# Kernel tuning notes

Hardware: AMD Instinct MI355X
Metric: run time of the kernel (lower is better)

## Reference

```python
import jax, jax.numpy as jnp
import numpy as np

H = 32  # hidden size
I = 6   # input size


def setup_inputs() -> dict:
    key = jax.random.key(0)
    ks = jax.random.split(key, 10)
    B, T = 8192, 256
    s_i = 1.0 / np.sqrt(H)  # PyTorch LSTM/Linear init scale (uniform), use normal*scale
    return {
        "x": jax.random.normal(ks[0], (B, T, I), dtype=jnp.float32),
        "W_ih": jax.random.normal(ks[1], (4 * H, I), dtype=jnp.float32) * s_i,
        "W_hh": jax.random.normal(ks[2], (4 * H, H), dtype=jnp.float32) * s_i,
        "b_ih": jax.random.normal(ks[3], (4 * H,), dtype=jnp.float32) * s_i,
        "b_hh": jax.random.normal(ks[4], (4 * H,), dtype=jnp.float32) * s_i,
        "W1": jax.random.normal(ks[5], (64, H), dtype=jnp.float32) * s_i,
        "b1": jax.random.normal(ks[6], (64,), dtype=jnp.float32) * s_i,
        "W2": jax.random.normal(ks[7], (1, 64), dtype=jnp.float32) * (1.0 / np.sqrt(64)),
        "b2": jax.random.normal(ks[8], (1,), dtype=jnp.float32) * (1.0 / np.sqrt(64)),
    }


def _lstm_last_h(x, W_ih, W_hh, b_ih, b_hh):
    # x: [B, T, I]. PyTorch gate order: i, f, g, o.
    B = x.shape[0]
    # Precompute input projections for all timesteps: [T, B, 4H]
    xg = jnp.einsum('bti,gi->tbg', x, W_ih) + (b_ih + b_hh)

    def step(carry, xg_t):
        h, c = carry
        gates = xg_t + h @ W_hh.T  # [B, 4H]
        i, f, g, o = jnp.split(gates, 4, axis=-1)
        i = jax.nn.sigmoid(i)
        f = jax.nn.sigmoid(f)
        g = jnp.tanh(g)
        o = jax.nn.sigmoid(o)
        c = f * c + i * g
        h = o * jnp.tanh(c)
        return (h, c), None

    h0 = jnp.zeros((B, H), dtype=x.dtype)
    c0 = jnp.zeros((B, H), dtype=x.dtype)
    (h_last, _), _ = jax.lax.scan(step, (h0, c0), xg)
    return h_last  # == lstm_out[:, -1, :]


def reference(x, W_ih, W_hh, b_ih, b_hh, W1, b1, W2, b2):
    h = _lstm_last_h(x, W_ih, W_hh, b_ih, b_hh)          # [B, 32]
    h = jax.nn.relu(h @ W1.T + b1)                        # [B, 64]
    return h @ W2.T + b2                                  # [B, 1]
```

## Files before the change

### kernel.cpp

```cpp
#include <hip/hip_runtime.h>
#include <cstdint>

#define HSZ 32
#define TSTEPS 256
#define ISZ 6
#define NB 16

typedef _Float16 h8_t __attribute__((ext_vector_type(8)));
typedef float f4_t __attribute__((ext_vector_type(4)));

#if __has_builtin(__builtin_amdgcn_exp2f)
__device__ __forceinline__ float exp2_raw(float x) { return __builtin_amdgcn_exp2f(x); }
#else
__device__ __forceinline__ float exp2_raw(float x) { return __expf(0.69314718056f * x); }
#endif

__global__ __launch_bounds__(64, 2) void lstm_wave(
    const float* __restrict__ x,
    const float* __restrict__ W_ih,
    const float* __restrict__ W_hh,
    const float* __restrict__ b_ih,
    const float* __restrict__ b_hh,
    const float* __restrict__ W1,
    const float* __restrict__ b1,
    const float* __restrict__ W2,
    const float* __restrict__ b2,
    float* __restrict__ out)
{
    __shared__ __align__(16) _Float16 hlds[NB][40];
    __shared__ float w1s[64 * 34];
    __shared__ float b1s[64];
    __shared__ float w2s[64];

    const int lane = threadIdx.x;
    const int n16  = lane & 15;
    const int khi  = lane >> 4;

    for (int i = lane; i < 64 * HSZ; i += 64) w1s[(i >> 5) * 34 + (i & 31)] = W1[i];
    b1s[lane] = b1[lane];
    w2s[lane] = W2[lane];
    #pragma unroll
    for (int i = 0; i < 5; ++i) ((unsigned int*)hlds)[lane + i * 64] = 0u;

    const float LOG2E = 1.44269504f;
    h8_t bhh[8], bih[8];
    f4_t bias4[8];
    #pragma unroll
    for (int q = 0; q < 8; ++q) {
        const int grow = q * 16 + n16;
        const float s = (q == 4 || q == 5) ? (-2.0f * LOG2E) : (-LOG2E);
        const float4* p = (const float4*)(W_hh + grow * HSZ + khi * 8);
        const float4 a = p[0], b = p[1];
        bhh[q][0] = (_Float16)(s * a.x); bhh[q][1] = (_Float16)(s * a.y);
        bhh[q][2] = (_Float16)(s * a.z); bhh[q][3] = (_Float16)(s * a.w);
        bhh[q][4] = (_Float16)(s * b.x); bhh[q][5] = (_Float16)(s * b.y);
        bhh[q][6] = (_Float16)(s * b.z); bhh[q][7] = (_Float16)(s * b.w);
        const float bb = s * (b_ih[grow] + b_hh[grow]);
        bias4[q][0] = bb; bias4[q][1] = bb; bias4[q][2] = bb; bias4[q][3] = bb;
        bih[q][0] = (_Float16)0; bih[q][1] = (_Float16)0;
        bih[q][2] = (_Float16)0; bih[q][3] = (_Float16)0;
        bih[q][4] = (_Float16)0; bih[q][5] = (_Float16)0;
        bih[q][6] = (_Float16)0; bih[q][7] = (_Float16)0;
        if (khi == 0) {
            const float2* pi = (const float2*)(W_ih + grow * ISZ);
            const float2 i0 = pi[0], i1 = pi[1], i2 = pi[2];
            bih[q][0] = (_Float16)(s * i0.x); bih[q][1] = (_Float16)(s * i0.y);
            bih[q][2] = (_Float16)(s * i1.x); bih[q][3] = (_Float16)(s * i1.y);
            bih[q][4] = (_Float16)(s * i2.x); bih[q][5] = (_Float16)(s * i2.y);
        }
    }

    const float* xb = x + (size_t)(blockIdx.x * NB + n16) * (TSTEPS * ISZ);
    float2 xa0 = ((const float2*)xb)[0], xa1 = ((const float2*)xb)[1], xa2 = ((const float2*)xb)[2];
    const float2* pn1 = (const float2*)(xb + ISZ);
    float2 xn0 = pn1[0], xn1 = pn1[1], xn2 = pn1[2];

    float c[2][4] = {{0.f, 0.f, 0.f, 0.f}, {0.f, 0.f, 0.f, 0.f}};

    __builtin_amdgcn_wave_barrier();

    for (int t = 0; t < TSTEPS; ++t) {
        const h8_t ah = *(const h8_t*)&hlds[n16][khi * 8];
        h8_t ax;
        ax[0] = (_Float16)xa0.x; ax[1] = (_Float16)xa0.y;
        ax[2] = (_Float16)xa1.x; ax[3] = (_Float16)xa1.y;
        ax[4] = (_Float16)xa2.x; ax[5] = (_Float16)xa2.y;
        ax[6] = (_Float16)0;     ax[7] = (_Float16)0;
        xa0 = xn0; xa1 = xn1; xa2 = xn2;
        const int tn = (t + 2 < TSTEPS) ? (t + 2) : (TSTEPS - 1);
        const float2* pn = (const float2*)(xb + tn * ISZ);
        xn0 = pn[0]; xn1 = pn[1]; xn2 = pn[2];

        f4_t d[8];
        #pragma unroll
        for (int q = 0; q < 8; ++q)
            d[q] = __builtin_amdgcn_mfma_f32_16x16x32_f16(ax, bih[q], bias4[q], 0, 0, 0);
        #pragma unroll
        for (int q = 0; q < 8; ++q)
            d[q] = __builtin_amdgcn_mfma_f32_16x16x32_f16(ah, bhh[q], d[q], 0, 0, 0);

        #pragma unroll
        for (int hh = 0; hh < 2; ++hh) {
            #pragma unroll
            for (int r = 0; r < 4; ++r) {
                const float iv = __builtin_amdgcn_rcpf(1.0f + exp2_raw(d[0 + hh][r]));
                const float fv = __builtin_amdgcn_rcpf(1.0f + exp2_raw(d[2 + hh][r]));
                const float gv = fmaf(2.0f, __builtin_amdgcn_rcpf(1.0f + exp2_raw(d[4 + hh][r])), -1.0f);
                const float ov = __builtin_amdgcn_rcpf(1.0f + exp2_raw(d[6 + hh][r]));
                c[hh][r] = fmaf(fv, c[hh][r], iv * gv);
                const float th = fmaf(2.0f, __builtin_amdgcn_rcpf(1.0f + exp2_raw(-2.88539008f * c[hh][r])), -1.0f);
                hlds[khi * 4 + r][hh * 16 + n16] = (_Float16)(ov * th);
            }
        }
        __builtin_amdgcn_wave_barrier();
    }

    __builtin_amdgcn_wave_barrier();
    float hr[32];
    #pragma unroll
    for (int q8 = 0; q8 < 4; ++q8) {
        const h8_t hv = *(const h8_t*)&hlds[n16][q8 * 8];
        #pragma unroll
        for (int e = 0; e < 8; ++e) hr[q8 * 8 + e] = (float)hv[e];
    }
    float rsum = 0.0f;
    #pragma unroll
    for (int u = 0; u < 16; ++u) {
        const int row = khi * 16 + u;
        float a = b1s[row];
        #pragma unroll
        for (int k = 0; k < 32; k += 2) {
            const float2 w = *(const float2*)&w1s[row * 34 + k];
            a = fmaf(w.x, hr[k], a);
            a = fmaf(w.y, hr[k + 1], a);
        }
        rsum = fmaf(fmaxf(a, 0.0f), w2s[row], rsum);
    }
    rsum += __shfl_xor(rsum, 16, 64);
    rsum += __shfl_xor(rsum, 32, 64);
    if (khi == 0) out[blockIdx.x * NB + n16] = rsum + b2[0];
}

extern "C" void kernel_launch(void* const* d_in, const int* in_sizes, int n_in,
                              void* d_out, int out_size, void* d_ws, size_t ws_size,
                              hipStream_t stream) {
    const float* x    = (const float*)d_in[0];
    const float* W_ih = (const float*)d_in[1];
    const float* W_hh = (const float*)d_in[2];
    const float* b_ih = (const float*)d_in[3];
    const float* b_hh = (const float*)d_in[4];
    const float* W1   = (const float*)d_in[5];
    const float* b1   = (const float*)d_in[6];
    const float* W2   = (const float*)d_in[7];
    const float* b2   = (const float*)d_in[8];
    float* out = (float*)d_out;

    const int B = in_sizes[0] / (TSTEPS * ISZ);
    const int grid = B / NB;

    lstm_wave<<<grid, 64, 0, stream>>>(x, W_ih, W_hh, b_ih, b_hh,
                                       W1, b1, W2, b2, out);
}
```

Measured before the change: 160.7 us.

## Fold bias into input MFMA, pipeline x-projection, merge sigmoid reciprocals

The combined bias is folded into the input-projection weights through a constant-one column in the x operand, which drops the per-gate bias accumulator registers. The x-projection MFMAs for the next timestep are issued after the gate math of the current one, so they sit off the h-dependent critical path. Sigmoid and tanh products are rewritten to share one reciprocal per pair, with exponents clamped to avoid overflow. This cuts transcendental count per step but adds fp16 rounding of the bias and extra clamp instructions.

```diff
diff --git a/kernel.cpp b/kernel.cpp
--- a/kernel.cpp
+++ b/kernel.cpp
@@ -14,6 +14,7 @@
 #else
 __device__ __forceinline__ float exp2_raw(float x) { return __expf(0.69314718056f * x); }
 #endif
+__device__ __forceinline__ float exp2c(float x) { return exp2_raw(fminf(x, 60.0f)); }
 
 __global__ __launch_bounds__(64, 2) void lstm_wave(
     const float* __restrict__ x,
@@ -44,7 +45,6 @@
 
     const float LOG2E = 1.44269504f;
     h8_t bhh[8], bih[8];
-    f4_t bias4[8];
     #pragma unroll
     for (int q = 0; q < 8; ++q) {
         const int grow = q * 16 + n16;
@@ -55,8 +55,6 @@
         bhh[q][2] = (_Float16)(s * a.z); bhh[q][3] = (_Float16)(s * a.w);
         bhh[q][4] = (_Float16)(s * b.x); bhh[q][5] = (_Float16)(s * b.y);
         bhh[q][6] = (_Float16)(s * b.z); bhh[q][7] = (_Float16)(s * b.w);
-        const float bb = s * (b_ih[grow] + b_hh[grow]);
-        bias4[q][0] = bb; bias4[q][1] = bb; bias4[q][2] = bb; bias4[q][3] = bb;
         bih[q][0] = (_Float16)0; bih[q][1] = (_Float16)0;
         bih[q][2] = (_Float16)0; bih[q][3] = (_Float16)0;
         bih[q][4] = (_Float16)0; bih[q][5] = (_Float16)0;
@@ -67,13 +65,29 @@
             bih[q][0] = (_Float16)(s * i0.x); bih[q][1] = (_Float16)(s * i0.y);
             bih[q][2] = (_Float16)(s * i1.x); bih[q][3] = (_Float16)(s * i1.y);
             bih[q][4] = (_Float16)(s * i2.x); bih[q][5] = (_Float16)(s * i2.y);
+            bih[q][6] = (_Float16)(s * (b_ih[grow] + b_hh[grow]));
         }
     }
 
     const float* xb = x + (size_t)(blockIdx.x * NB + n16) * (TSTEPS * ISZ);
-    float2 xa0 = ((const float2*)xb)[0], xa1 = ((const float2*)xb)[1], xa2 = ((const float2*)xb)[2];
-    const float2* pn1 = (const float2*)(xb + ISZ);
-    float2 xn0 = pn1[0], xn1 = pn1[1], xn2 = pn1[2];
+    float2 xn0 = ((const float2*)xb)[0], xn1 = ((const float2*)xb)[1], xn2 = ((const float2*)xb)[2];
+
+    const f4_t zf = {0.f, 0.f, 0.f, 0.f};
+    h8_t ax;
+    ax[0] = (_Float16)xn0.x; ax[1] = (_Float16)xn0.y;
+    ax[2] = (_Float16)xn1.x; ax[3] = (_Float16)xn1.y;
+    ax[4] = (_Float16)xn2.x; ax[5] = (_Float16)xn2.y;
+    ax[6] = (_Float16)1;     ax[7] = (_Float16)0;
+
+    f4_t dx[8];
+    #pragma unroll
+    for (int q = 0; q < 8; ++q)
+        dx[q] = __builtin_amdgcn_mfma_f32_16x16x32_f16(ax, bih[q], zf, 0, 0, 0);
+
+    {
+        const float2* pn = (const float2*)(xb + ISZ);
+        xn0 = pn[0]; xn1 = pn[1]; xn2 = pn[2];
+    }
 
     float c[2][4] = {{0.f, 0.f, 0.f, 0.f}, {0.f, 0.f, 0.f, 0.f}};
 
@@ -81,37 +95,39 @@
 
     for (int t = 0; t < TSTEPS; ++t) {
         const h8_t ah = *(const h8_t*)&hlds[n16][khi * 8];
-        h8_t ax;
-        ax[0] = (_Float16)xa0.x; ax[1] = (_Float16)xa0.y;
-        ax[2] = (_Float16)xa1.x; ax[3] = (_Float16)xa1.y;
-        ax[4] = (_Float16)xa2.x; ax[5] = (_Float16)xa2.y;
-        ax[6] = (_Float16)0;     ax[7] = (_Float16)0;
-        xa0 = xn0; xa1 = xn1; xa2 = xn2;
-        const int tn = (t + 2 < TSTEPS) ? (t + 2) : (TSTEPS - 1);
-        const float2* pn = (const float2*)(xb + tn * ISZ);
-        xn0 = pn[0]; xn1 = pn[1]; xn2 = pn[2];
-
         f4_t d[8];
         #pragma unroll
         for (int q = 0; q < 8; ++q)
-            d[q] = __builtin_amdgcn_mfma_f32_16x16x32_f16(ax, bih[q], bias4[q], 0, 0, 0);
-        #pragma unroll
-        for (int q = 0; q < 8; ++q)
-            d[q] = __builtin_amdgcn_mfma_f32_16x16x32_f16(ah, bhh[q], d[q], 0, 0, 0);
+            d[q] = __builtin_amdgcn_mfma_f32_16x16x32_f16(ah, bhh[q], dx[q], 0, 0, 0);
 
         #pragma unroll
         for (int hh = 0; hh < 2; ++hh) {
             #pragma unroll
             for (int r = 0; r < 4; ++r) {
-                const float iv = __builtin_amdgcn_rcpf(1.0f + exp2_raw(d[0 + hh][r]));
-                const float fv = __builtin_amdgcn_rcpf(1.0f + exp2_raw(d[2 + hh][r]));
-                const float gv = fmaf(2.0f, __builtin_amdgcn_rcpf(1.0f + exp2_raw(d[4 + hh][r])), -1.0f);
-                const float ov = __builtin_amdgcn_rcpf(1.0f + exp2_raw(d[6 + hh][r]));
-                c[hh][r] = fmaf(fv, c[hh][r], iv * gv);
-                const float th = fmaf(2.0f, __builtin_amdgcn_rcpf(1.0f + exp2_raw(-2.88539008f * c[hh][r])), -1.0f);
-                hlds[khi * 4 + r][hh * 16 + n16] = (_Float16)(ov * th);
+                const float ei = exp2c(d[0 + hh][r]);
+                const float ef = exp2c(d[2 + hh][r]);
+                const float eg = exp2c(d[4 + hh][r]);
+                const float eo = exp2c(d[6 + hh][r]);
+                const float fv = __builtin_amdgcn_rcpf(1.0f + ef);
+                const float ig = (1.0f - eg) * __builtin_amdgcn_rcpf((1.0f + ei) * (1.0f + eg));
+                c[hh][r] = fmaf(fv, c[hh][r], ig);
+                const float ec = exp2c(-2.88539008f * c[hh][r]);
+                const float hv = (1.0f - ec) * __builtin_amdgcn_rcpf((1.0f + eo) * (1.0f + ec));
+                hlds[khi * 4 + r][hh * 16 + n16] = (_Float16)hv;
             }
         }
+
+        ax[0] = (_Float16)xn0.x; ax[1] = (_Float16)xn0.y;
+        ax[2] = (_Float16)xn1.x; ax[3] = (_Float16)xn1.y;
+        ax[4] = (_Float16)xn2.x; ax[5] = (_Float16)xn2.y;
+        #pragma unroll
+        for (int q = 0; q < 8; ++q)
+            dx[q] = __builtin_amdgcn_mfma_f32_16x16x32_f16(ax, bih[q], zf, 0, 0, 0);
+
+        const int tn = (t + 2 < TSTEPS) ? (t + 2) : (TSTEPS - 1);
+        const float2* pn = (const float2*)(xb + tn * ISZ);
+        xn0 = pn[0]; xn1 = pn[1]; xn2 = pn[2];
+
         __builtin_amdgcn_wave_barrier();
     }
 
```

Result: slower. 186.7 us (+16.2%).

## Split LSTM hidden units across two waves with double-buffered LDS state

Applied to the files above, without the earlier changes.

Each block now runs two wavefronts, and each wave computes the gates for half of the 32 hidden units. That halves the MFMA and transcendental work per wave on the serial recurrence and doubles the number of active waves. The hidden state is double-buffered in LDS and exchanged with a block barrier every timestep. The gate nonlinearities are also reworked so that i*g and o*tanh(c) each use a single reciprocal, with exp2 inputs clamped to avoid overflow. The cost is a __syncthreads per step and the risk of lower occupancy per CU.

```diff
diff --git a/kernel.cpp b/kernel.cpp
--- a/kernel.cpp
+++ b/kernel.cpp
@@ -14,8 +14,9 @@
 #else
 __device__ __forceinline__ float exp2_raw(float x) { return __expf(0.69314718056f * x); }
 #endif
+__device__ __forceinline__ float exp2c(float x) { return exp2_raw(fminf(x, 60.0f)); }
 
-__global__ __launch_bounds__(64, 2) void lstm_wave(
+__global__ __launch_bounds__(128, 1) void lstm_split(
     const float* __restrict__ x,
     const float* __restrict__ W_ih,
     const float* __restrict__ W_hh,
@@ -27,46 +28,46 @@
     const float* __restrict__ b2,
     float* __restrict__ out)
 {
-    __shared__ __align__(16) _Float16 hlds[NB][40];
+    __shared__ __align__(16) _Float16 hlds[2][NB][40];
     __shared__ float w1s[64 * 34];
     __shared__ float b1s[64];
     __shared__ float w2s[64];
 
-    const int lane = threadIdx.x;
+    const int tid  = threadIdx.x;
+    const int uh   = tid >> 6;
+    const int lane = tid & 63;
     const int n16  = lane & 15;
     const int khi  = lane >> 4;
 
-    for (int i = lane; i < 64 * HSZ; i += 64) w1s[(i >> 5) * 34 + (i & 31)] = W1[i];
-    b1s[lane] = b1[lane];
-    w2s[lane] = W2[lane];
-    #pragma unroll
-    for (int i = 0; i < 5; ++i) ((unsigned int*)hlds)[lane + i * 64] = 0u;
+    for (int i = tid; i < 64 * HSZ; i += 128) w1s[(i >> 5) * 34 + (i & 31)] = W1[i];
+    if (tid < 64) { b1s[tid] = b1[tid]; w2s[tid] = W2[tid]; }
+    for (int i = tid; i < (NB * 40) / 2; i += 128) ((unsigned int*)hlds)[i] = 0u;
 
     const float LOG2E = 1.44269504f;
-    h8_t bhh[8], bih[8];
-    f4_t bias4[8];
+    h8_t bhh[4], bih[4];
+    f4_t bias4[4];
     #pragma unroll
-    for (int q = 0; q < 8; ++q) {
-        const int grow = q * 16 + n16;
-        const float s = (q == 4 || q == 5) ? (-2.0f * LOG2E) : (-LOG2E);
+    for (int g = 0; g < 4; ++g) {
+        const int grow = g * 32 + uh * 16 + n16;
+        const float s = (g == 2) ? (-2.0f * LOG2E) : (-LOG2E);
         const float4* p = (const float4*)(W_hh + grow * HSZ + khi * 8);
         const float4 a = p[0], b = p[1];
-        bhh[q][0] = (_Float16)(s * a.x); bhh[q][1] = (_Float16)(s * a.y);
-        bhh[q][2] = (_Float16)(s * a.z); bhh[q][3] = (_Float16)(s * a.w);
-        bhh[q][4] = (_Float16)(s * b.x); bhh[q][5] = (_Float16)(s * b.y);
-        bhh[q][6] = (_Float16)(s * b.z); bhh[q][7] = (_Float16)(s * b.w);
+        bhh[g][0] = (_Float16)(s * a.x); bhh[g][1] = (_Float16)(s * a.y);
+        bhh[g][2] = (_Float16)(s * a.z); bhh[g][3] = (_Float16)(s * a.w);
+        bhh[g][4] = (_Float16)(s * b.x); bhh[g][5] = (_Float16)(s * b.y);
+        bhh[g][6] = (_Float16)(s * b.z); bhh[g][7] = (_Float16)(s * b.w);
         const float bb = s * (b_ih[grow] + b_hh[grow]);
-        bias4[q][0] = bb; bias4[q][1] = bb; bias4[q][2] = bb; bias4[q][3] = bb;
-        bih[q][0] = (_Float16)0; bih[q][1] = (_Float16)0;
-        bih[q][2] = (_Float16)0; bih[q][3] = (_Float16)0;
-        bih[q][4] = (_Float16)0; bih[q][5] = (_Float16)0;
-        bih[q][6] = (_Float16)0; bih[q][7] = (_Float16)0;
+        bias4[g][0] = bb; bias4[g][1] = bb; bias4[g][2] = bb; bias4[g][3] = bb;
+        bih[g][0] = (_Float16)0; bih[g][1] = (_Float16)0;
+        bih[g][2] = (_Float16)0; bih[g][3] = (_Float16)0;
+        bih[g][4] = (_Float16)0; bih[g][5] = (_Float16)0;
+        bih[g][6] = (_Float16)0; bih[g][7] = (_Float16)0;
         if (khi == 0) {
             const float2* pi = (const float2*)(W_ih + grow * ISZ);
             const float2 i0 = pi[0], i1 = pi[1], i2 = pi[2];
-            bih[q][0] = (_Float16)(s * i0.x); bih[q][1] = (_Float16)(s * i0.y);
-            bih[q][2] = (_Float16)(s * i1.x); bih[q][3] = (_Float16)(s * i1.y);
-            bih[q][4] = (_Float16)(s * i2.x); bih[q][5] = (_Float16)(s * i2.y);
+            bih[g][0] = (_Float16)(s * i0.x); bih[g][1] = (_Float16)(s * i0.y);
+            bih[g][2] = (_Float16)(s * i1.x); bih[g][3] = (_Float16)(s * i1.y);
+            bih[g][4] = (_Float16)(s * i2.x); bih[g][5] = (_Float16)(s * i2.y);
         }
     }
 
@@ -75,12 +76,12 @@
     const float2* pn1 = (const float2*)(xb + ISZ);
     float2 xn0 = pn1[0], xn1 = pn1[1], xn2 = pn1[2];
 
-    float c[2][4] = {{0.f, 0.f, 0.f, 0.f}, {0.f, 0.f, 0.f, 0.f}};
+    float c[4] = {0.f, 0.f, 0.f, 0.f};
 
-    __builtin_amdgcn_wave_barrier();
+    __syncthreads();
 
     for (int t = 0; t < TSTEPS; ++t) {
-        const h8_t ah = *(const h8_t*)&hlds[n16][khi * 8];
+        const h8_t ah = *(const h8_t*)&hlds[t & 1][n16][khi * 8];
         h8_t ax;
         ax[0] = (_Float16)xa0.x; ax[1] = (_Float16)xa0.y;
         ax[2] = (_Float16)xa1.x; ax[3] = (_Float16)xa1.y;
@@ -91,54 +92,56 @@
         const float2* pn = (const float2*)(xb + tn * ISZ);
         xn0 = pn[0]; xn1 = pn[1]; xn2 = pn[2];
 
-        f4_t d[8];
+        f4_t d[4];
         #pragma unroll
-        for (int q = 0; q < 8; ++q)
-            d[q] = __builtin_amdgcn_mfma_f32_16x16x32_f16(ax, bih[q], bias4[q], 0, 0, 0);
+        for (int g = 0; g < 4; ++g)
+            d[g] = __builtin_amdgcn_mfma_f32_16x16x32_f16(ax, bih[g], bias4[g], 0, 0, 0);
         #pragma unroll
-        for (int q = 0; q < 8; ++q)
-            d[q] = __builtin_amdgcn_mfma_f32_16x16x32_f16(ah, bhh[q], d[q], 0, 0, 0);
+        for (int g = 0; g < 4; ++g)
+            d[g] = __builtin_amdgcn_mfma_f32_16x16x32_f16(ah, bhh[g], d[g], 0, 0, 0);
 
+        const int wb = (t + 1) & 1;
         #pragma unroll
-        for (int hh = 0; hh < 2; ++hh) {
-            #pragma unroll
-            for (int r = 0; r < 4; ++r) {
-                const float iv = __builtin_amdgcn_rcpf(1.0f + exp2_raw(d[0 + hh][r]));
-                const float fv = __builtin_amdgcn_rcpf(1.0f + exp2_raw(d[2 + hh][r]));
-                const float gv = fmaf(2.0f, __builtin_amdgcn_rcpf(1.0f + exp2_raw(d[4 + hh][r])), -1.0f);
-                const float ov = __builtin_amdgcn_rcpf(1.0f + exp2_raw(d[6 + hh][r]));
-                c[hh][r] = fmaf(fv, c[hh][r], iv * gv);
-                const float th = fmaf(2.0f, __builtin_amdgcn_rcpf(1.0f + exp2_raw(-2.88539008f * c[hh][r])), -1.0f);
-                hlds[khi * 4 + r][hh * 16 + n16] = (_Float16)(ov * th);
-            }
+        for (int r = 0; r < 4; ++r) {
+            const float ei = exp2c(d[0][r]);
+            const float ef = exp2c(d[1][r]);
+            const float eg = exp2c(d[2][r]);
+            const float eo = exp2c(d[3][r]);
+            const float fv = __builtin_amdgcn_rcpf(1.0f + ef);
+            const float ig = (1.0f - eg) * __builtin_amdgcn_rcpf((1.0f + ei) * (1.0f + eg));
+            c[r] = fmaf(fv, c[r], ig);
+            const float ec = exp2c(-2.88539008f * c[r]);
+            const float hv = (1.0f - ec) * __builtin_amdgcn_rcpf((1.0f + eo) * (1.0f + ec));
+            hlds[wb][khi * 4 + r][uh * 16 + n16] = (_Float16)hv;
         }
-        __builtin_amdgcn_wave_barrier();
+        __syncthreads();
     }
 
-    __builtin_amdgcn_wave_barrier();
-    float hr[32];
-    #pragma unroll
-    for (int q8 = 0; q8 < 4; ++q8) {
-        const h8_t hv = *(const h8_t*)&hlds[n16][q8 * 8];
+    if (uh == 0) {
+        float hr[32];
         #pragma unroll
-        for (int e = 0; e < 8; ++e) hr[q8 * 8 + e] = (float)hv[e];
+        for (int q8 = 0; q8 < 4; ++q8) {
+            const h8_t hv = *(const h8_t*)&hlds[0][n16][q8 * 8];
+            #pragma unroll
+            for (int e = 0; e < 8; ++e) hr[q8 * 8 + e] = (float)hv[e];
+        }
+        float rsum = 0.0f;
+        #pragma unroll
+        for (int u = 0; u < 16; ++u) {
+            const int row = khi * 16 + u;
+            float a = b1s[row];
+            #pragma unroll
+            for (int k = 0; k < 32; k += 2) {
+                const float2 w = *(const float2*)&w1s[row * 34 + k];
+                a = fmaf(w.x, hr[k], a);
+                a = fmaf(w.y, hr[k + 1], a);
+            }
+            rsum = fmaf(fmaxf(a, 0.0f), w2s[row], rsum);
+        }
+        rsum += __shfl_xor(rsum, 16, 64);
+        rsum += __shfl_xor(rsum, 32, 64);
+        if (khi == 0) out[blockIdx.x * NB + n16] = rsum + b2[0];
     }
-    float rsum = 0.0f;
-    #pragma unroll
-    for (int u = 0; u < 16; ++u) {
-        const int row = khi * 16 + u;
-        float a = b1s[row];
-        #pragma unroll
-        for (int k = 0; k < 32; k += 2) {
-            const float2 w = *(const float2*)&w1s[row * 34 + k];
-            a = fmaf(w.x, hr[k], a);
-            a = fmaf(w.y, hr[k + 1], a);
-        }
-        rsum = fmaf(fmaxf(a, 0.0f), w2s[row], rsum);
-    }
-    rsum += __shfl_xor(rsum, 16, 64);
-    rsum += __shfl_xor(rsum, 32, 64);
-    if (khi == 0) out[blockIdx.x * NB + n16] = rsum + b2[0];
 }
 
 extern "C" void kernel_launch(void* const* d_in, const int* in_sizes, int n_in,
@@ -158,6 +161,6 @@
     const int B = in_sizes[0] / (TSTEPS * ISZ);
     const int grid = B / NB;
 
-    lstm_wave<<<grid, 64, 0, stream>>>(x, W_ih, W_hh, b_ih, b_hh,
-                                       W1, b1, W2, b2, out);
+    lstm_split<<<grid, 128, 0, stream>>>(x, W_ih, W_hh, b_ih, b_hh,
+                                         W1, b1, W2, b2, out);
 }
```

Measured after the change: 197.2 us. 22.7% more time.

## Stage x in LDS as fp16, fold bias into MFMA, merge gate reciprocals

Applied to the files above, without the earlier changes.

Before the recurrence, the block's whole input sequence is copied into shared memory as fp16, replacing the per-step global prefetch with LDS reads. The combined bias moves into the input-weight operand through a constant-1 input lane, so the accumulators start at zero and the bias4 registers go away. The gate nonlinearities are rewritten to share denominators, cutting each element's five reciprocals to two. The added LDS footprint of about 24KB lowers occupancy (launch bounds now allow 1 block), and both the fp16 bias and the merged-denominator form add rounding and overflow risk.

```diff
diff --git a/kernel.cpp b/kernel.cpp
--- a/kernel.cpp
+++ b/kernel.cpp
@@ -6,6 +6,8 @@
 #define ISZ 6
 #define NB 16
 
+typedef _Float16 h2_t __attribute__((ext_vector_type(2)));
+typedef _Float16 h4_t __attribute__((ext_vector_type(4)));
 typedef _Float16 h8_t __attribute__((ext_vector_type(8)));
 typedef float f4_t __attribute__((ext_vector_type(4)));
 
@@ -15,7 +17,7 @@
 __device__ __forceinline__ float exp2_raw(float x) { return __expf(0.69314718056f * x); }
 #endif
 
-__global__ __launch_bounds__(64, 2) void lstm_wave(
+__global__ __launch_bounds__(64, 1) void lstm_wave(
     const float* __restrict__ x,
     const float* __restrict__ W_ih,
     const float* __restrict__ W_hh,
@@ -27,6 +29,8 @@
     const float* __restrict__ b2,
     float* __restrict__ out)
 {
+    __shared__ __align__(8) _Float16 xs2[TSTEPS][NB][4];
+    __shared__ __align__(4) _Float16 xs1[TSTEPS][NB][2];
     __shared__ __align__(16) _Float16 hlds[NB][40];
     __shared__ float w1s[64 * 34];
     __shared__ float b1s[64];
@@ -36,6 +40,19 @@
     const int n16  = lane & 15;
     const int khi  = lane >> 4;
 
+    {
+        const float* xg = x + (size_t)blockIdx.x * (NB * TSTEPS * ISZ);
+        for (int i = lane; i < NB * TSTEPS; i += 64) {
+            const int b = i >> 8, t = i & 255;
+            const float2* p = (const float2*)(xg + ((size_t)b * TSTEPS + t) * ISZ);
+            const float2 v0 = p[0], v1 = p[1], v2 = p[2];
+            h4_t lo; lo[0] = (_Float16)v0.x; lo[1] = (_Float16)v0.y;
+                     lo[2] = (_Float16)v1.x; lo[3] = (_Float16)v1.y;
+            h2_t hi; hi[0] = (_Float16)v2.x; hi[1] = (_Float16)v2.y;
+            *(h4_t*)&xs2[t][b][0] = lo;
+            *(h2_t*)&xs1[t][b][0] = hi;
+        }
+    }
     for (int i = lane; i < 64 * HSZ; i += 64) w1s[(i >> 5) * 34 + (i & 31)] = W1[i];
     b1s[lane] = b1[lane];
     w2s[lane] = W2[lane];
@@ -44,7 +61,6 @@
 
     const float LOG2E = 1.44269504f;
     h8_t bhh[8], bih[8];
-    f4_t bias4[8];
     #pragma unroll
     for (int q = 0; q < 8; ++q) {
         const int grow = q * 16 + n16;
@@ -55,8 +71,6 @@
         bhh[q][2] = (_Float16)(s * a.z); bhh[q][3] = (_Float16)(s * a.w);
         bhh[q][4] = (_Float16)(s * b.x); bhh[q][5] = (_Float16)(s * b.y);
         bhh[q][6] = (_Float16)(s * b.z); bhh[q][7] = (_Float16)(s * b.w);
-        const float bb = s * (b_ih[grow] + b_hh[grow]);
-        bias4[q][0] = bb; bias4[q][1] = bb; bias4[q][2] = bb; bias4[q][3] = bb;
         bih[q][0] = (_Float16)0; bih[q][1] = (_Float16)0;
         bih[q][2] = (_Float16)0; bih[q][3] = (_Float16)0;
         bih[q][4] = (_Float16)0; bih[q][5] = (_Float16)0;
@@ -67,34 +81,28 @@
             bih[q][0] = (_Float16)(s * i0.x); bih[q][1] = (_Float16)(s * i0.y);
             bih[q][2] = (_Float16)(s * i1.x); bih[q][3] = (_Float16)(s * i1.y);
             bih[q][4] = (_Float16)(s * i2.x); bih[q][5] = (_Float16)(s * i2.y);
+            bih[q][6] = (_Float16)(s * (b_ih[grow] + b_hh[grow]));
         }
     }
 
-    const float* xb = x + (size_t)(blockIdx.x * NB + n16) * (TSTEPS * ISZ);
-    float2 xa0 = ((const float2*)xb)[0], xa1 = ((const float2*)xb)[1], xa2 = ((const float2*)xb)[2];
-    const float2* pn1 = (const float2*)(xb + ISZ);
-    float2 xn0 = pn1[0], xn1 = pn1[1], xn2 = pn1[2];
-
     float c[2][4] = {{0.f, 0.f, 0.f, 0.f}, {0.f, 0.f, 0.f, 0.f}};
+    const f4_t zf = {0.f, 0.f, 0.f, 0.f};
 
     __builtin_amdgcn_wave_barrier();
 
     for (int t = 0; t < TSTEPS; ++t) {
-        const h8_t ah = *(const h8_t*)&hlds[n16][khi * 8];
+        const h8_t ah  = *(const h8_t*)&hlds[n16][khi * 8];
+        const h4_t xlo = *(const h4_t*)&xs2[t][n16][0];
+        const h2_t xhi = *(const h2_t*)&xs1[t][n16][0];
         h8_t ax;
-        ax[0] = (_Float16)xa0.x; ax[1] = (_Float16)xa0.y;
-        ax[2] = (_Float16)xa1.x; ax[3] = (_Float16)xa1.y;
-        ax[4] = (_Float16)xa2.x; ax[5] = (_Float16)xa2.y;
-        ax[6] = (_Float16)0;     ax[7] = (_Float16)0;
-        xa0 = xn0; xa1 = xn1; xa2 = xn2;
-        const int tn = (t + 2 < TSTEPS) ? (t + 2) : (TSTEPS - 1);
-        const float2* pn = (const float2*)(xb + tn * ISZ);
-        xn0 = pn[0]; xn1 = pn[1]; xn2 = pn[2];
+        ax[0] = xlo[0]; ax[1] = xlo[1]; ax[2] = xlo[2]; ax[3] = xlo[3];
+        ax[4] = xhi[0]; ax[5] = xhi[1];
+        ax[6] = (_Float16)1; ax[7] = (_Float16)0;
 
         f4_t d[8];
         #pragma unroll
         for (int q = 0; q < 8; ++q)
-            d[q] = __builtin_amdgcn_mfma_f32_16x16x32_f16(ax, bih[q], bias4[q], 0, 0, 0);
+            d[q] = __builtin_amdgcn_mfma_f32_16x16x32_f16(ax, bih[q], zf, 0, 0, 0);
         #pragma unroll
         for (int q = 0; q < 8; ++q)
             d[q] = __builtin_amdgcn_mfma_f32_16x16x32_f16(ah, bhh[q], d[q], 0, 0, 0);
@@ -103,13 +111,17 @@
         for (int hh = 0; hh < 2; ++hh) {
             #pragma unroll
             for (int r = 0; r < 4; ++r) {
-                const float iv = __builtin_amdgcn_rcpf(1.0f + exp2_raw(d[0 + hh][r]));
-                const float fv = __builtin_amdgcn_rcpf(1.0f + exp2_raw(d[2 + hh][r]));
-                const float gv = fmaf(2.0f, __builtin_amdgcn_rcpf(1.0f + exp2_raw(d[4 + hh][r])), -1.0f);
-                const float ov = __builtin_amdgcn_rcpf(1.0f + exp2_raw(d[6 + hh][r]));
-                c[hh][r] = fmaf(fv, c[hh][r], iv * gv);
-                const float th = fmaf(2.0f, __builtin_amdgcn_rcpf(1.0f + exp2_raw(-2.88539008f * c[hh][r])), -1.0f);
-                hlds[khi * 4 + r][hh * 16 + n16] = (_Float16)(ov * th);
+                const float ei = exp2_raw(d[0 + hh][r]);
+                const float ef = exp2_raw(d[2 + hh][r]);
+                const float eg = exp2_raw(d[4 + hh][r]);
+                const float eo = exp2_raw(d[6 + hh][r]);
+                const float pf  = 1.0f + ef;
+                const float pig = (1.0f + ei) * (1.0f + eg);
+                const float num = fmaf(c[hh][r], pig, (1.0f - eg) * pf);
+                c[hh][r] = num * __builtin_amdgcn_rcpf(pf * pig);
+                const float ec = exp2_raw(-2.88539008f * c[hh][r]);
+                const float hv = (1.0f - ec) * __builtin_amdgcn_rcpf((1.0f + eo) * (1.0f + ec));
+                hlds[khi * 4 + r][hh * 16 + n16] = (_Float16)hv;
             }
         }
         __builtin_amdgcn_wave_barrier();
```

After: 178.0 us. 10.8% more time.
